# Kernel optimization log

Measured on AMD Instinct MI355X. Metric: run time of the kernel, lower is better.

The kernel has to match this reference:

```python
import jax, jax.numpy as jnp
import numpy as np

NUM_SAMPLES = 128  # from __init__ default


def _trilinear_sample(vox, g):
    """grid_sample 5D, mode=bilinear (trilinear), padding_mode=zeros, align_corners=True.
    vox: [C, Dv, Hv, Wv]; g: [P, 3] normalized (x,y,z) with x->Wv, y->Hv, z->Dv.
    Returns [P, C]."""
    C, D, Hh, Ww = vox.shape
    x = (g[:, 0] + 1.0) * 0.5 * (Ww - 1)
    y = (g[:, 1] + 1.0) * 0.5 * (Hh - 1)
    z = (g[:, 2] + 1.0) * 0.5 * (D - 1)
    x0 = jnp.floor(x); y0 = jnp.floor(y); z0 = jnp.floor(z)
    xd = x - x0; yd = y - y0; zd = z - z0
    x0i = x0.astype(jnp.int32); y0i = y0.astype(jnp.int32); z0i = z0.astype(jnp.int32)
    out = jnp.zeros((g.shape[0], C), vox.dtype)
    for dz, wz in ((0, 1.0 - zd), (1, zd)):
        for dy, wy in ((0, 1.0 - yd), (1, yd)):
            for dx, wx in ((0, 1.0 - xd), (1, xd)):
                zi = z0i + dz; yi = y0i + dy; xi = x0i + dx
                valid = ((zi >= 0) & (zi < D) & (yi >= 0) & (yi < Hh) & (xi >= 0) & (xi < Ww)).astype(vox.dtype)
                zc = jnp.clip(zi, 0, D - 1); yc = jnp.clip(yi, 0, Hh - 1); xc = jnp.clip(xi, 0, Ww - 1)
                vals = vox[:, zc, yc, xc]  # [C, P]
                out = out + ((wz * wy * wx * valid)[:, None]) * vals.T
    return out


def setup_inputs() -> dict:
    key = jax.random.key(0)
    k1, k2 = jax.random.split(key)
    B, Hv, Wv, Dv = 4, 128, 128, 128
    H, W = 128, 128
    rgbsigma = jax.random.uniform(k1, (B, Hv, Wv, Dv, 4), dtype=jnp.float32)
    # cameras at ~z=3 looking down -z (identity rotation), slightly jittered
    pose = jnp.tile(jnp.eye(4, dtype=jnp.float32), (B, 1, 1))
    trans = jnp.array([0.0, 0.0, 3.0], dtype=jnp.float32) + 0.1 * jax.random.normal(k2, (B, 3), dtype=jnp.float32)
    pose = pose.at[:, :3, 3].set(trans)
    K = jnp.tile(jnp.array([[150.0, 0.0, 64.0], [0.0, 150.0, 64.0], [0.0, 0.0, 1.0]], dtype=jnp.float32), (B, 1, 1))
    bbox_min = jnp.tile(jnp.array([-1.0, -1.0, -1.0], dtype=jnp.float32), (B, 1))
    bbox_max = jnp.tile(jnp.array([1.0, 1.0, 1.0], dtype=jnp.float32), (B, 1))
    return {"rgbsigma": rgbsigma, "camera_pose": pose, "camera_intrinsics": K,
            "bbox_min": bbox_min, "bbox_max": bbox_max, "H": H, "W": W}


def reference(rgbsigma, camera_pose, camera_intrinsics, bbox_min, bbox_max, H, W):
    B = camera_pose.shape[0]
    N = H * W
    # --- ray generation ---
    ii, jj = jnp.meshgrid(jnp.arange(H, dtype=jnp.float32), jnp.arange(W, dtype=jnp.float32), indexing='ij')
    ii = ii.reshape(-1); jj = jj.reshape(-1)  # [N]
    fx = camera_intrinsics[:, 0, 0][:, None]; fy = camera_intrinsics[:, 1, 1][:, None]
    cx = camera_intrinsics[:, 0, 2][:, None]; cy = camera_intrinsics[:, 1, 2][:, None]
    dirs = jnp.stack([(jj[None, :] - cx) / fx, -(ii[None, :] - cy) / fy,
                      -jnp.ones((B, N), dtype=jnp.float32)], axis=-1)  # [B,N,3]
    rays_d = jnp.einsum('bij,bnj->bni', camera_pose[:, :3, :3], dirs)
    rays_d = rays_d / jnp.maximum(jnp.linalg.norm(rays_d, axis=-1, keepdims=True), 1e-12)
    rays_o = jnp.broadcast_to(camera_pose[:, None, :3, 3], (B, N, 3))
    # --- near/far via slab test ---
    inv_d = 1.0 / (rays_d + 1e-10)
    bmin = bbox_min[:, None, :]; bmax = bbox_max[:, None, :]
    t_min = (bmin - rays_o) * inv_d; t_max = (bmax - rays_o) * inv_d
    t1 = jnp.minimum(t_min, t_max); t2 = jnp.maximum(t_min, t_max)
    near = jnp.maximum(jnp.max(t1, axis=-1, keepdims=True), 0.1)
    far = jnp.maximum(jnp.min(t2, axis=-1, keepdims=True), near + 0.1)
    # --- stratified-uniform sample points ---
    t_vals = jnp.linspace(0.0, 1.0, NUM_SAMPLES, dtype=jnp.float32)
    z_vals = near + (far - near) * t_vals  # [B,N,M]
    pts = rays_o[:, :, None, :] + rays_d[:, :, None, :] * z_vals[..., None]  # [B,N,M,3]
    # --- trilinear voxel query ---
    scale = (bbox_max - bbox_min + 1e-10)[:, None, None, :]
    pts_norm = 2.0 * (pts - bbox_min[:, None, None, :]) / scale - 1.0
    vox = jnp.transpose(rgbsigma, (0, 4, 3, 1, 2))  # [B,4,Dv,Hv,Wv]
    sampled = jax.vmap(_trilinear_sample)(vox, pts_norm.reshape(B, N * NUM_SAMPLES, 3))
    sampled = sampled.reshape(B, N, NUM_SAMPLES, 4)
    rgb = sampled[..., :3]; sigma = sampled[..., 3]
    # --- alpha compositing ---
    dists = z_vals[..., 1:] - z_vals[..., :-1]
    dists = jnp.concatenate([dists, jnp.full_like(dists[..., :1], 1e10)], axis=-1)
    alpha = 1.0 - jnp.exp(-jax.nn.relu(sigma) * dists)
    trans = jnp.cumprod(jnp.concatenate([jnp.ones_like(alpha[..., :1]), 1.0 - alpha + 1e-10], axis=-1), axis=-1)[..., :-1]
    weights = alpha * trans
    rgb_map = jnp.sum(weights[..., None] * rgb, axis=-2)  # [B,N,3]
    acc_map = jnp.sum(weights, axis=-1)
    rgb_map = rgb_map + (1.0 - acc_map[..., None])  # white background
    return jnp.transpose(rgb_map.reshape(B, H, W, 3), (0, 3, 1, 2))
```

## Files before the change

### kernel.cpp

```cpp
#include <hip/hip_runtime.h>

#define NSAMP 128
#define VD 128
#define WPB 4

struct Corner8 {
    float4 v0, v1, v2, v3, v4, v5, v6, v7;
    float  w0, w1, w2, w3, w4, w5, w6, w7;
};

__device__ __forceinline__ void compute_ray_setup(
    int ray, int N, int W,
    const float* __restrict__ pose, const float* __restrict__ Kmat,
    const float* __restrict__ bmin, const float* __restrict__ bmax,
    float& axv, float& bxv, float& ayv, float& byv, float& azv, float& bzv,
    float& near, float& dt)
{
    const int b = ray / N;
    const int pix = ray - b * N;
    const int i = pix / W;
    const int j = pix - i * W;

    const float* P  = pose + b * 16;
    const float* Kb = Kmat + b * 9;
    const float fx = Kb[0], cx = Kb[2], fy = Kb[4], cy = Kb[5];

    const float dcx = ((float)j - cx) / fx;
    const float dcy = -((float)i - cy) / fy;
    const float dcz = -1.0f;

    float dx = P[0]*dcx + P[1]*dcy + P[2]*dcz;
    float dy = P[4]*dcx + P[5]*dcy + P[6]*dcz;
    float dz = P[8]*dcx + P[9]*dcy + P[10]*dcz;
    float nrm = sqrtf(dx*dx + dy*dy + dz*dz);
    nrm = fmaxf(nrm, 1e-12f);
    dx /= nrm; dy /= nrm; dz /= nrm;

    const float ox = P[3], oy = P[7], oz = P[11];

    const float bx0 = bmin[b*3+0], by0 = bmin[b*3+1], bz0 = bmin[b*3+2];
    const float bx1 = bmax[b*3+0], by1 = bmax[b*3+1], bz1 = bmax[b*3+2];

    const float ivx = 1.0f / (dx + 1e-10f);
    const float ivy = 1.0f / (dy + 1e-10f);
    const float ivz = 1.0f / (dz + 1e-10f);

    float ta, tb;
    ta = (bx0 - ox) * ivx; tb = (bx1 - ox) * ivx;
    const float t1x = fminf(ta, tb), t2x = fmaxf(ta, tb);
    ta = (by0 - oy) * ivy; tb = (by1 - oy) * ivy;
    const float t1y = fminf(ta, tb), t2y = fmaxf(ta, tb);
    ta = (bz0 - oz) * ivz; tb = (bz1 - oz) * ivz;
    const float t1z = fminf(ta, tb), t2z = fmaxf(ta, tb);

    near = fmaxf(fmaxf(t1x, fmaxf(t1y, t1z)), 0.1f);
    const float far = fmaxf(fminf(t2x, fminf(t2y, t2z)), near + 0.1f);

    const float sxs = (bx1 - bx0) + 1e-10f;
    const float sys = (by1 - by0) + 1e-10f;
    const float szs = (bz1 - bz0) + 1e-10f;
    const float C = (float)(VD - 1);
    axv = (ox - bx0) / sxs * C; bxv = dx / sxs * C;
    ayv = (oy - by0) / sys * C; byv = dy / sys * C;
    azv = (oz - bz0) / szs * C; bzv = dz / szs * C;

    dt = (far - near) * (1.0f / (float)(NSAMP - 1));
}

__global__ __launch_bounds__(256)
void RaySetup_kernel(const float* __restrict__ pose,
                     const float* __restrict__ Kmat,
                     const float* __restrict__ bmin,
                     const float* __restrict__ bmax,
                     const int* __restrict__ dH,
                     const int* __restrict__ dW,
                     float* __restrict__ rp,
                     int rays)
{
    const int ray = blockIdx.x * blockDim.x + threadIdx.x;
    if (ray >= rays) return;
    const int H = dH[0], W = dW[0];
    const int N = H * W;
    float axv, bxv, ayv, byv, azv, bzv, near, dt;
    compute_ray_setup(ray, N, W, pose, Kmat, bmin, bmax,
                      axv, bxv, ayv, byv, azv, bzv, near, dt);
    float4* o = reinterpret_cast<float4*>(rp + (size_t)ray * 8);
    o[0] = make_float4(axv, bxv, ayv, byv);
    o[1] = make_float4(azv, bzv, near, dt);
}

__device__ __forceinline__ void fetch_sample(
    Corner8& Bf, const float4* __restrict__ V4, float t,
    float axv, float bxv, float ayv, float byv, float azv, float bzv)
{
    const float xf = axv + bxv * t;
    const float yf = ayv + byv * t;
    const float zf = azv + bzv * t;
    const float x0f = floorf(xf), y0f = floorf(yf), z0f = floorf(zf);
    const float xd = xf - x0f, yd = yf - y0f, zd = zf - z0f;
    const int x0 = (int)x0f, y0 = (int)y0f, z0 = (int)z0f;
    const int x1 = x0 + 1, y1 = y0 + 1, z1 = z0 + 1;

    const int xc0 = min(max(x0, 0), VD - 1), xc1 = min(max(x1, 0), VD - 1);
    const int yc0 = min(max(y0, 0), VD - 1), yc1 = min(max(y1, 0), VD - 1);
    const int zc0 = min(max(z0, 0), VD - 1), zc1 = min(max(z1, 0), VD - 1);

    const float vx0 = (x0 == xc0) ? 1.0f : 0.0f;
    const float vx1 = (x1 == xc1) ? 1.0f : 0.0f;
    const float vy0 = (y0 == yc0) ? 1.0f : 0.0f;
    const float vy1 = (y1 == yc1) ? 1.0f : 0.0f;
    const float vz0 = (z0 == zc0) ? 1.0f : 0.0f;
    const float vz1 = (z1 == zc1) ? 1.0f : 0.0f;

    const float wx0 = (1.0f - xd) * vx0, wx1 = xd * vx1;
    const float wy0 = (1.0f - yd) * vy0, wy1 = yd * vy1;
    const float wz0 = (1.0f - zd) * vz0, wz1 = zd * vz1;

    const int r0 = yc0 << 14, r1 = yc1 << 14;
    const int c0 = xc0 << 7,  c1 = xc1 << 7;
    const int i00 = r0 + c0, i01 = r0 + c1;
    const int i10 = r1 + c0, i11 = r1 + c1;

    Bf.v0 = V4[i00 + zc0];
    Bf.v1 = V4[i00 + zc1];
    Bf.v2 = V4[i01 + zc0];
    Bf.v3 = V4[i01 + zc1];
    Bf.v4 = V4[i10 + zc0];
    Bf.v5 = V4[i10 + zc1];
    Bf.v6 = V4[i11 + zc0];
    Bf.v7 = V4[i11 + zc1];

    Bf.w0 = wy0 * wx0 * wz0;
    Bf.w1 = wy0 * wx0 * wz1;
    Bf.w2 = wy0 * wx1 * wz0;
    Bf.w3 = wy0 * wx1 * wz1;
    Bf.w4 = wy1 * wx0 * wz0;
    Bf.w5 = wy1 * wx0 * wz1;
    Bf.w6 = wy1 * wx1 * wz0;
    Bf.w7 = wy1 * wx1 * wz1;
}

__device__ __forceinline__ float4 interp_sample(const Corner8& Bf)
{
    float4 r;
    r.x = Bf.w0*Bf.v0.x + Bf.w1*Bf.v1.x + Bf.w2*Bf.v2.x + Bf.w3*Bf.v3.x
        + Bf.w4*Bf.v4.x + Bf.w5*Bf.v5.x + Bf.w6*Bf.v6.x + Bf.w7*Bf.v7.x;
    r.y = Bf.w0*Bf.v0.y + Bf.w1*Bf.v1.y + Bf.w2*Bf.v2.y + Bf.w3*Bf.v3.y
        + Bf.w4*Bf.v4.y + Bf.w5*Bf.v5.y + Bf.w6*Bf.v6.y + Bf.w7*Bf.v7.y;
    r.z = Bf.w0*Bf.v0.z + Bf.w1*Bf.v1.z + Bf.w2*Bf.v2.z + Bf.w3*Bf.v3.z
        + Bf.w4*Bf.v4.z + Bf.w5*Bf.v5.z + Bf.w6*Bf.v6.z + Bf.w7*Bf.v7.z;
    r.w = Bf.w0*Bf.v0.w + Bf.w1*Bf.v1.w + Bf.w2*Bf.v2.w + Bf.w3*Bf.v3.w
        + Bf.w4*Bf.v4.w + Bf.w5*Bf.v5.w + Bf.w6*Bf.v6.w + Bf.w7*Bf.v7.w;
    return r;
}

__device__ __forceinline__ float scan_prod64(float v, int lane)
{
    #pragma unroll
    for (int d = 1; d < 64; d <<= 1) {
        const float o = __shfl_up(v, d, 64);
        if (lane >= d) v *= o;
    }
    return v;
}

template <bool USE_WS>
__global__ __launch_bounds__(256, 1)
void VoxelRenderer_kernel(const float* __restrict__ vol,
                          const float* __restrict__ pose,
                          const float* __restrict__ Kmat,
                          const float* __restrict__ bmin,
                          const float* __restrict__ bmax,
                          const int* __restrict__ dH,
                          const int* __restrict__ dW,
                          const float* __restrict__ rayp,
                          float* __restrict__ out,
                          int rays)
{
    const int lane = threadIdx.x & 63;
    const int wid  = threadIdx.x >> 6;

    const int nwg = gridDim.x;
    const int bid = blockIdx.x;
    const int q = nwg >> 3, r = nwg & 7;
    const int xcd = bid & 7, idx = bid >> 3;
    const int swz = (xcd < r ? xcd * (q + 1) : r * (q + 1) + (xcd - r) * q) + idx;

    const int ray = swz * WPB + wid;
    if (ray >= rays) return;

    const int H = dH[0], W = dW[0];
    const int N = H * W;
    const int b = ray / N;
    const int pix = ray - b * N;

    float axv, bxv, ayv, byv, azv, bzv, near, dt;
    if (USE_WS) {
        const float4* p = reinterpret_cast<const float4*>(rayp + (size_t)ray * 8);
        const float4 p0 = p[0];
        const float4 p1 = p[1];
        axv = p0.x; bxv = p0.y; ayv = p0.z; byv = p0.w;
        azv = p1.x; bzv = p1.y; near = p1.z; dt = p1.w;
    } else {
        compute_ray_setup(ray, N, W, pose, Kmat, bmin, bmax,
                          axv, bxv, ayv, byv, azv, bzv, near, dt);
    }

    const float4* __restrict__ V4 =
        reinterpret_cast<const float4*>(vol + (size_t)b * VD * VD * VD * 4);

    const float tA = near + dt * (float)lane;
    const float tB = near + dt * (float)(lane + 64);

    Corner8 A, Bf;
    fetch_sample(A,  V4, tA, axv, bxv, ayv, byv, azv, bzv);
    fetch_sample(Bf, V4, tB, axv, bxv, ayv, byv, azv, bzv);

    const float4 sA = interp_sample(A);
    const float sigA = fmaxf(sA.w, 0.0f);
    const float alphaA = 1.0f - __expf(-sigA * dt);
    const float tmA = 1.0f - alphaA + 1e-10f;

    float inclA = scan_prod64(tmA, lane);
    float PA = __shfl_up(inclA, 1, 64);
    if (lane == 0) PA = 1.0f;
    const float TtotA = __shfl(inclA, 63, 64);

    const float4 sB = interp_sample(Bf);
    const float sigB = fmaxf(sB.w, 0.0f);
    const float distB = (lane == 63) ? 1e10f : dt;
    const float alphaB = 1.0f - __expf(-sigB * distB);
    const float tmB = 1.0f - alphaB + 1e-10f;

    float inclB = scan_prod64(tmB, lane);
    float PB = __shfl_up(inclB, 1, 64);
    if (lane == 0) PB = 1.0f;

    const float wA = alphaA * PA;
    const float wB = alphaB * PB * TtotA;

    float R  = wA * sA.x + wB * sB.x;
    float G  = wA * sA.y + wB * sB.y;
    float Bl = wA * sA.z + wB * sB.z;
    float Aw = wA + wB;

    #pragma unroll
    for (int d = 1; d < 64; d <<= 1) {
        R  += __shfl_xor(R,  d, 64);
        G  += __shfl_xor(G,  d, 64);
        Bl += __shfl_xor(Bl, d, 64);
        Aw += __shfl_xor(Aw, d, 64);
    }

    if (lane == 0) {
        const float bg = 1.0f - Aw;
        float* outb = out + (size_t)b * 3 * N + pix;
        outb[0 * (size_t)N] = R + bg;
        outb[1 * (size_t)N] = G + bg;
        outb[2 * (size_t)N] = Bl + bg;
    }
}

extern "C" void kernel_launch(void* const* d_in, const int* in_sizes, int n_in,
                              void* d_out, int out_size, void* d_ws, size_t ws_size,
                              hipStream_t stream) {
    const float* rgbsigma = (const float*)d_in[0];
    const float* pose     = (const float*)d_in[1];
    const float* Kmat     = (const float*)d_in[2];
    const float* bmin     = (const float*)d_in[3];
    const float* bmax     = (const float*)d_in[4];
    const int*   dH       = (const int*)d_in[5];
    const int*   dW       = (const int*)d_in[6];
    float* out = (float*)d_out;

    const int rays = out_size / 3;
    const int grid = (rays + WPB - 1) / WPB;
    const bool use_ws = ws_size >= (size_t)rays * 8 * sizeof(float);

    if (use_ws) {
        float* rp = (float*)d_ws;
        RaySetup_kernel<<<(rays + 255) / 256, 256, 0, stream>>>(
            pose, Kmat, bmin, bmax, dH, dW, rp, rays);
        VoxelRenderer_kernel<true><<<grid, 64 * WPB, 0, stream>>>(
            rgbsigma, pose, Kmat, bmin, bmax, dH, dW, rp, out, rays);
    } else {
        VoxelRenderer_kernel<false><<<grid, 64 * WPB, 0, stream>>>(
            rgbsigma, pose, Kmat, bmin, bmax, dH, dW, nullptr, out, rays);
    }
}
```

Before: 66.19 us.

## Split each ray's samples across two wavefronts and combine via shared memory

Each ray now uses two wavefronts, each handling 64 of the 128 samples. Each computes its partial composite and transmittance, and the two are merged through shared memory after a block barrier. The aim is to double the number of wavefronts in flight so gather latency is hidden better and per-thread register pressure drops. In exchange it adds a __syncthreads, a shared-memory exchange, duplicated ray setup per half, and 512-thread blocks. The interpolation sums are also reassociated into pairs to shorten dependency chains.

```diff
diff --git a/kernel.cpp b/kernel.cpp
--- a/kernel.cpp
+++ b/kernel.cpp
@@ -143,14 +143,14 @@
 __device__ __forceinline__ float4 interp_sample(const Corner8& Bf)
 {
     float4 r;
-    r.x = Bf.w0*Bf.v0.x + Bf.w1*Bf.v1.x + Bf.w2*Bf.v2.x + Bf.w3*Bf.v3.x
-        + Bf.w4*Bf.v4.x + Bf.w5*Bf.v5.x + Bf.w6*Bf.v6.x + Bf.w7*Bf.v7.x;
-    r.y = Bf.w0*Bf.v0.y + Bf.w1*Bf.v1.y + Bf.w2*Bf.v2.y + Bf.w3*Bf.v3.y
-        + Bf.w4*Bf.v4.y + Bf.w5*Bf.v5.y + Bf.w6*Bf.v6.y + Bf.w7*Bf.v7.y;
-    r.z = Bf.w0*Bf.v0.z + Bf.w1*Bf.v1.z + Bf.w2*Bf.v2.z + Bf.w3*Bf.v3.z
-        + Bf.w4*Bf.v4.z + Bf.w5*Bf.v5.z + Bf.w6*Bf.v6.z + Bf.w7*Bf.v7.z;
-    r.w = Bf.w0*Bf.v0.w + Bf.w1*Bf.v1.w + Bf.w2*Bf.v2.w + Bf.w3*Bf.v3.w
-        + Bf.w4*Bf.v4.w + Bf.w5*Bf.v5.w + Bf.w6*Bf.v6.w + Bf.w7*Bf.v7.w;
+    r.x = (Bf.w0*Bf.v0.x + Bf.w1*Bf.v1.x) + (Bf.w2*Bf.v2.x + Bf.w3*Bf.v3.x)
+        + (Bf.w4*Bf.v4.x + Bf.w5*Bf.v5.x) + (Bf.w6*Bf.v6.x + Bf.w7*Bf.v7.x);
+    r.y = (Bf.w0*Bf.v0.y + Bf.w1*Bf.v1.y) + (Bf.w2*Bf.v2.y + Bf.w3*Bf.v3.y)
+        + (Bf.w4*Bf.v4.y + Bf.w5*Bf.v5.y) + (Bf.w6*Bf.v6.y + Bf.w7*Bf.v7.y);
+    r.z = (Bf.w0*Bf.v0.z + Bf.w1*Bf.v1.z) + (Bf.w2*Bf.v2.z + Bf.w3*Bf.v3.z)
+        + (Bf.w4*Bf.v4.z + Bf.w5*Bf.v5.z) + (Bf.w6*Bf.v6.z + Bf.w7*Bf.v7.z);
+    r.w = (Bf.w0*Bf.v0.w + Bf.w1*Bf.v1.w) + (Bf.w2*Bf.v2.w + Bf.w3*Bf.v3.w)
+        + (Bf.w4*Bf.v4.w + Bf.w5*Bf.v5.w) + (Bf.w6*Bf.v6.w + Bf.w7*Bf.v7.w);
     return r;
 }
 
@@ -165,7 +165,7 @@
 }
 
 template <bool USE_WS>
-__global__ __launch_bounds__(256, 1)
+__global__ __launch_bounds__(512, 1)
 void VoxelRenderer_kernel(const float* __restrict__ vol,
                           const float* __restrict__ pose,
                           const float* __restrict__ Kmat,
@@ -179,6 +179,8 @@
 {
     const int lane = threadIdx.x & 63;
     const int wid  = threadIdx.x >> 6;
+    const int rib  = wid >> 1;
+    const int half = wid & 1;
 
     const int nwg = gridDim.x;
     const int bid = blockIdx.x;
@@ -186,78 +188,91 @@
     const int xcd = bid & 7, idx = bid >> 3;
     const int swz = (xcd < r ? xcd * (q + 1) : r * (q + 1) + (xcd - r) * q) + idx;
 
-    const int ray = swz * WPB + wid;
-    if (ray >= rays) return;
+    const int ray = swz * WPB + rib;
 
     const int H = dH[0], W = dW[0];
     const int N = H * W;
-    const int b = ray / N;
-    const int pix = ray - b * N;
-
-    float axv, bxv, ayv, byv, azv, bzv, near, dt;
-    if (USE_WS) {
-        const float4* p = reinterpret_cast<const float4*>(rayp + (size_t)ray * 8);
-        const float4 p0 = p[0];
-        const float4 p1 = p[1];
-        axv = p0.x; bxv = p0.y; ayv = p0.z; byv = p0.w;
-        azv = p1.x; bzv = p1.y; near = p1.z; dt = p1.w;
-    } else {
-        compute_ray_setup(ray, N, W, pose, Kmat, bmin, bmax,
-                          axv, bxv, ayv, byv, azv, bzv, near, dt);
+
+    __shared__ float s_res[2 * WPB][5];
+
+    if (ray < rays) {
+        const int b = ray / N;
+
+        float axv, bxv, ayv, byv, azv, bzv, near, dt;
+        if (USE_WS) {
+            const float4* p = reinterpret_cast<const float4*>(rayp + (size_t)ray * 8);
+            const float4 p0 = p[0];
+            const float4 p1 = p[1];
+            axv = p0.x; bxv = p0.y; ayv = p0.z; byv = p0.w;
+            azv = p1.x; bzv = p1.y; near = p1.z; dt = p1.w;
+        } else {
+            compute_ray_setup(ray, N, W, pose, Kmat, bmin, bmax,
+                              axv, bxv, ayv, byv, azv, bzv, near, dt);
+        }
+
+        const float4* __restrict__ V4 =
+            reinterpret_cast<const float4*>(vol + (size_t)b * VD * VD * VD * 4);
+
+        const int k = half * 64 + lane;
+        const float t = near + dt * (float)k;
+
+        Corner8 A;
+        fetch_sample(A, V4, t, axv, bxv, ayv, byv, azv, bzv);
+
+        const float4 s = interp_sample(A);
+        const float sig = fmaxf(s.w, 0.0f);
+        const float dist = (k == NSAMP - 1) ? 1e10f : dt;
+        const float alpha = 1.0f - __expf(-sig * dist);
+        const float tm = 1.0f - alpha + 1e-10f;
+
+        const float incl = scan_prod64(tm, lane);
+        float P = __shfl_up(incl, 1, 64);
+        if (lane == 0) P = 1.0f;
+        const float Ttot = __shfl(incl, 63, 64);
+
+        const float w = alpha * P;
+        float R  = w * s.x;
+        float G  = w * s.y;
+        float Bl = w * s.z;
+        float Aw = w;
+
+        #pragma unroll
+        for (int d = 1; d < 64; d <<= 1) {
+            R  += __shfl_xor(R,  d, 64);
+            G  += __shfl_xor(G,  d, 64);
+            Bl += __shfl_xor(Bl, d, 64);
+            Aw += __shfl_xor(Aw, d, 64);
+        }
+
+        if (lane == 0) {
+            s_res[wid][0] = R;
+            s_res[wid][1] = G;
+            s_res[wid][2] = Bl;
+            s_res[wid][3] = Aw;
+            s_res[wid][4] = Ttot;
+        }
     }
 
-    const float4* __restrict__ V4 =
-        reinterpret_cast<const float4*>(vol + (size_t)b * VD * VD * VD * 4);
-
-    const float tA = near + dt * (float)lane;
-    const float tB = near + dt * (float)(lane + 64);
-
-    Corner8 A, Bf;
-    fetch_sample(A,  V4, tA, axv, bxv, ayv, byv, azv, bzv);
-    fetch_sample(Bf, V4, tB, axv, bxv, ayv, byv, azv, bzv);
-
-    const float4 sA = interp_sample(A);
-    const float sigA = fmaxf(sA.w, 0.0f);
-    const float alphaA = 1.0f - __expf(-sigA * dt);
-    const float tmA = 1.0f - alphaA + 1e-10f;
-
-    float inclA = scan_prod64(tmA, lane);
-    float PA = __shfl_up(inclA, 1, 64);
-    if (lane == 0) PA = 1.0f;
-    const float TtotA = __shfl(inclA, 63, 64);
-
-    const float4 sB = interp_sample(Bf);
-    const float sigB = fmaxf(sB.w, 0.0f);
-    const float distB = (lane == 63) ? 1e10f : dt;
-    const float alphaB = 1.0f - __expf(-sigB * distB);
-    const float tmB = 1.0f - alphaB + 1e-10f;
-
-    float inclB = scan_prod64(tmB, lane);
-    float PB = __shfl_up(inclB, 1, 64);
-    if (lane == 0) PB = 1.0f;
-
-    const float wA = alphaA * PA;
-    const float wB = alphaB * PB * TtotA;
-
-    float R  = wA * sA.x + wB * sB.x;
-    float G  = wA * sA.y + wB * sB.y;
-    float Bl = wA * sA.z + wB * sB.z;
-    float Aw = wA + wB;
-
-    #pragma unroll
-    for (int d = 1; d < 64; d <<= 1) {
-        R  += __shfl_xor(R,  d, 64);
-        G  += __shfl_xor(G,  d, 64);
-        Bl += __shfl_xor(Bl, d, 64);
-        Aw += __shfl_xor(Aw, d, 64);
-    }
-
-    if (lane == 0) {
-        const float bg = 1.0f - Aw;
-        float* outb = out + (size_t)b * 3 * N + pix;
-        outb[0 * (size_t)N] = R + bg;
-        outb[1 * (size_t)N] = G + bg;
-        outb[2 * (size_t)N] = Bl + bg;
+    __syncthreads();
+
+    if (threadIdx.x < WPB) {
+        const int r2 = swz * WPB + threadIdx.x;
+        if (r2 < rays) {
+            const float* h0 = s_res[threadIdx.x * 2];
+            const float* h1 = s_res[threadIdx.x * 2 + 1];
+            const float T0 = h0[4];
+            const float R  = h0[0] + T0 * h1[0];
+            const float G  = h0[1] + T0 * h1[1];
+            const float Bl = h0[2] + T0 * h1[2];
+            const float Aw = h0[3] + T0 * h1[3];
+            const float bg = 1.0f - Aw;
+            const int b2 = r2 / N;
+            const int pix2 = r2 - b2 * N;
+            float* outb = out + (size_t)b2 * 3 * N + pix2;
+            outb[0 * (size_t)N] = R + bg;
+            outb[1 * (size_t)N] = G + bg;
+            outb[2 * (size_t)N] = Bl + bg;
+        }
     }
 }
 
@@ -281,10 +296,10 @@
         float* rp = (float*)d_ws;
         RaySetup_kernel<<<(rays + 255) / 256, 256, 0, stream>>>(
             pose, Kmat, bmin, bmax, dH, dW, rp, rays);
-        VoxelRenderer_kernel<true><<<grid, 64 * WPB, 0, stream>>>(
+        VoxelRenderer_kernel<true><<<grid, 128 * WPB, 0, stream>>>(
             rgbsigma, pose, Kmat, bmin, bmax, dH, dW, rp, out, rays);
     } else {
-        VoxelRenderer_kernel<false><<<grid, 64 * WPB, 0, stream>>>(
+        VoxelRenderer_kernel<false><<<grid, 128 * WPB, 0, stream>>>(
             rgbsigma, pose, Kmat, bmin, bmax, dH, dW, nullptr, out, rays);
     }
 }
```

Result: slower. 75.07 us (+13.4%).
